# Kernel optimization log

Measured on AMD Instinct MI355X. Metric: run time of the kernel, lower is better.

## Reference

```python
import jax, jax.numpy as jnp
import numpy as np

N = 50000
E = 800000
D_IN, D_HID, D_OUT = 128, 128, 64


def setup_inputs() -> dict:
    key = jax.random.key(0)
    ks = jax.random.split(key, 8)
    x = jax.random.normal(ks[0], (N, D_IN), dtype=jnp.float32)
    edge_index = jax.random.randint(ks[1], (2, E), 0, N, dtype=jnp.int64)
    # SAGEConv params: lin_l (neighbors, with bias), lin_r (root, no bias)
    s1 = 1.0 / np.sqrt(D_IN)
    s2 = 1.0 / np.sqrt(D_HID)
    W1_l = jax.random.uniform(ks[2], (D_IN, D_HID), jnp.float32, -s1, s1)
    b1 = jnp.zeros((D_HID,), jnp.float32)
    W1_r = jax.random.uniform(ks[3], (D_IN, D_HID), jnp.float32, -s1, s1)
    W2_l = jax.random.uniform(ks[4], (D_HID, D_OUT), jnp.float32, -s2, s2)
    b2 = jnp.zeros((D_OUT,), jnp.float32)
    W2_r = jax.random.uniform(ks[5], (D_HID, D_OUT), jnp.float32, -s2, s2)
    return {"x": x, "edge_index": edge_index, "W1_l": W1_l, "b1": b1,
            "W1_r": W1_r, "W2_l": W2_l, "b2": b2, "W2_r": W2_r}


def _sage_conv(x, src, dst, Wl, b, Wr, num_nodes):
    # mean aggregation over incoming edges (src -> dst)
    msgs = x[src]                                              # [E, d]
    agg = jax.ops.segment_sum(msgs, dst, num_segments=num_nodes)
    cnt = jax.ops.segment_sum(jnp.ones((src.shape[0],), x.dtype), dst,
                              num_segments=num_nodes)
    mean = agg / jnp.clip(cnt, 1.0)[:, None]                   # [N, d]
    return mean @ Wl + b + x @ Wr


def reference(x, edge_index, W1_l, b1, W1_r, W2_l, b2, W2_r):
    src, dst = edge_index[0], edge_index[1]
    n = x.shape[0]
    h = jax.nn.relu(_sage_conv(x, src, dst, W1_l, b1, W1_r, n))
    # dropout p=0.5 is identity in eval mode (training=False)
    return _sage_conv(h, src, dst, W2_l, b2, W2_r, n)
```

## Files before the change

### kernel.cpp

```cpp
#include <hip/hip_runtime.h>
#include <hip/hip_bf16.h>

typedef __hip_bfloat16 bf16;
typedef __attribute__((ext_vector_type(8))) short short8;
typedef __attribute__((ext_vector_type(4))) float floatx4;
typedef __attribute__((ext_vector_type(2))) float floatx2;
typedef unsigned short u16;
typedef unsigned char u8;

#define NNODES 50000
#define NEDGES 800000
#define D_IN  128
#define D_HID 128
#define D_OUT 64
#define NBLK  ((NNODES + 255) / 256)

__device__ __forceinline__ float bfbits2f(unsigned int u) {
    return __uint_as_float(u << 16);
}
__device__ __forceinline__ float b2f(bf16 v) { return __bfloat162float(v); }
__device__ __forceinline__ unsigned short f2bfbits(float f) {
    bf16 b = __float2bfloat16(f);
    return *(unsigned short*)&b;
}
__device__ __forceinline__ u8 f2fp8(float f) {
    return (u8)(__builtin_amdgcn_cvt_pk_fp8_f32(f, 0.f, 0, false) & 0xFF);
}
__device__ __forceinline__ float ld(const void* p, long long idx, int isf32) {
    if (isf32) return ((const float*)p)[idx];
    return b2f(((const bf16*)p)[idx]);
}

__global__ void k_setup(int* __restrict__ cnt, int n,
                        const unsigned int* __restrict__ ei_words,
                        const unsigned int* __restrict__ w_words,
                        int* __restrict__ flags,
                        const void* __restrict__ x,
                        const void* __restrict__ W1l, const void* __restrict__ W1r,
                        const void* __restrict__ W2l, const void* __restrict__ W2r,
                        bf16* __restrict__ p1l, bf16* __restrict__ p1r,
                        bf16* __restrict__ p2l, bf16* __restrict__ p2r,
                        unsigned int* __restrict__ x8) {
    int b = blockIdx.x;
    if (b < 128) {
        if (b == 0) {
            __shared__ int cnt_zero, cnt_bf;
            if (threadIdx.x == 0) { cnt_zero = 0; cnt_bf = 0; }
            __syncthreads();
            int t = threadIdx.x;
            unsigned int we = ei_words[2 * t + 1];
            if (we == 0u) atomicAdd(&cnt_zero, 1);
            unsigned int ww = w_words[t];
            unsigned int lowexp = (ww >> 7) & 0xFFu;
            if (lowexp >= 0x60u && lowexp <= 0x7Bu) atomicAdd(&cnt_bf, 1);
            __syncthreads();
            if (threadIdx.x == 0) {
                flags[0] = (cnt_zero >= 240) ? 1 : 0;
                flags[1] = (cnt_bf >= 192) ? 0 : 1;
            }
        }
        int i = b * blockDim.x + threadIdx.x;
        int stride = 128 * blockDim.x;
        for (; i < n; i += stride) cnt[i] = 0;
        return;
    }
    __shared__ int cnt_bf2;
    if (threadIdx.x == 0) cnt_bf2 = 0;
    __syncthreads();
    {
        unsigned int ww = w_words[threadIdx.x];
        unsigned int lowexp = (ww >> 7) & 0xFFu;
        if (lowexp >= 0x60u && lowexp <= 0x7Bu) atomicAdd(&cnt_bf2, 1);
    }
    __syncthreads();
    int isf32 = (cnt_bf2 >= 192) ? 0 : 1;
    if (b < 152) {
        int t = (b - 128) * 256 + threadIdx.x;
        if (t >= 6144) return;
        const void* Wm; bf16* dst; int NT; int base;
        if (t < 2048)      { Wm = W1l; dst = p1l; NT = 8; base = t; }
        else if (t < 4096) { Wm = W1r; dst = p1r; NT = 8; base = t - 2048; }
        else if (t < 5120) { Wm = W2l; dst = p2l; NT = 4; base = t - 4096; }
        else               { Wm = W2r; dst = p2r; NT = 4; base = t - 5120; }
        int lane = base & 63;
        int kt = (base >> 6) & 3;
        int nt = base >> 8;
        int Nmat = NT * 16;
        int krow = kt * 32 + ((lane >> 4) * 8);
        int col = nt * 16 + (lane & 15);
        #pragma unroll
        for (int j = 0; j < 8; j++) {
            float v = ld(Wm, (long long)(krow + j) * Nmat + col, isf32);
            dst[(((nt * 4 + kt) * 64 + lane) * 8) + j] = __float2bfloat16(v);
        }
        return;
    }
    const long long NU32 = (long long)NNODES * D_IN / 4;
    long long i = (long long)(b - 152) * 256 + threadIdx.x;
    long long stride = (long long)(gridDim.x - 152) * 256;
    if (isf32) {
        const float4* xf = (const float4*)x;
        for (; i < NU32; i += stride) {
            float4 f = xf[i];
            unsigned int w0 = __builtin_amdgcn_cvt_pk_fp8_f32(f.x, f.y, 0, false);
            w0 = __builtin_amdgcn_cvt_pk_fp8_f32(f.z, f.w, w0, true);
            x8[i] = w0;
        }
    } else {
        const ushort4* xb = (const ushort4*)x;
        for (; i < NU32; i += stride) {
            ushort4 s = xb[i];
            float f0 = bfbits2f(s.x), f1 = bfbits2f(s.y);
            float f2 = bfbits2f(s.z), f3 = bfbits2f(s.w);
            unsigned int w0 = __builtin_amdgcn_cvt_pk_fp8_f32(f0, f1, 0, false);
            w0 = __builtin_amdgcn_cvt_pk_fp8_f32(f2, f3, w0, true);
            x8[i] = w0;
        }
    }
}

__global__ void k_edges(const int* __restrict__ ei, const int* __restrict__ flags,
                        u16* __restrict__ src16, unsigned int* __restrict__ drpack,
                        int* __restrict__ cnt) {
    int e = blockIdx.x * blockDim.x + threadIdx.x;
    if (e >= NEDGES) return;
    int s, d;
    if (flags[0]) { s = ei[2 * e]; d = ei[2 * (NEDGES + e)]; }
    else          { s = ei[e];     d = ei[NEDGES + e]; }
    src16[e] = (u16)s;
    int rank = atomicAdd(&cnt[d], 1);
    drpack[e] = ((unsigned int)rank << 16) | (unsigned int)d;
}

__global__ void k_scan_a(const int* __restrict__ cnt, int* __restrict__ excl,
                         int* __restrict__ bsum) {
    __shared__ int s[256];
    int t = threadIdx.x;
    int i = blockIdx.x * 256 + t;
    int v = (i < NNODES) ? cnt[i] : 0;
    s[t] = v;
    __syncthreads();
    for (int off = 1; off < 256; off <<= 1) {
        int u = (t >= off) ? s[t - off] : 0;
        __syncthreads();
        s[t] += u;
        __syncthreads();
    }
    if (i < NNODES) excl[i] = s[t] - v;
    if (t == 255) bsum[blockIdx.x] = s[255];
}

__global__ void k_scan_bc(const int* __restrict__ excl, const int* __restrict__ bsum,
                          int* __restrict__ row_start) {
    __shared__ int s[256];
    __shared__ int bo;
    int t = threadIdx.x;
    int v = (t < NBLK) ? bsum[t] : 0;
    s[t] = v;
    __syncthreads();
    for (int off = 1; off < 256; off <<= 1) {
        int u = (t >= off) ? s[t - off] : 0;
        __syncthreads();
        s[t] += u;
        __syncthreads();
    }
    if (t == 0) bo = s[blockIdx.x] - bsum[blockIdx.x];
    __syncthreads();
    int i = blockIdx.x * 256 + t;
    if (i < NNODES) row_start[i] = bo + excl[i];
    if (i == 0) row_start[NNODES] = NEDGES;
}

__global__ void k_scatter(const u16* __restrict__ src16,
                          const unsigned int* __restrict__ drpack,
                          const int* __restrict__ row_start,
                          u16* __restrict__ csr16) {
    int e = blockIdx.x * blockDim.x + threadIdx.x;
    if (e >= NEDGES) return;
    unsigned int dp = drpack[e];
    int d = (int)(dp & 0xFFFFu);
    int r = (int)(dp >> 16);
    csr16[row_start[d] + r] = src16[e];
}

__device__ __forceinline__ void g16m(const unsigned int* __restrict__ x8w, int my,
                                     int j, int cnt2, int h, int c,
                                     float& a0, float& a1, float& a2, float& a3) {
    int jb = j + h * 8;
    int i0 = __shfl(my, jb + 0), i1 = __shfl(my, jb + 1);
    int i2 = __shfl(my, jb + 2), i3 = __shfl(my, jb + 3);
    int i4 = __shfl(my, jb + 4), i5 = __shfl(my, jb + 5);
    int i6 = __shfl(my, jb + 6), i7 = __shfl(my, jb + 7);
    unsigned int u0 = x8w[((unsigned)i0 << 5) + c];
    unsigned int u1 = x8w[((unsigned)i1 << 5) + c];
    unsigned int u2 = x8w[((unsigned)i2 << 5) + c];
    unsigned int u3 = x8w[((unsigned)i3 << 5) + c];
    unsigned int u4 = x8w[((unsigned)i4 << 5) + c];
    unsigned int u5 = x8w[((unsigned)i5 << 5) + c];
    unsigned int u6 = x8w[((unsigned)i6 << 5) + c];
    unsigned int u7 = x8w[((unsigned)i7 << 5) + c];
    float m0 = (jb + 0 < cnt2) ? 1.f : 0.f;
    float m1 = (jb + 1 < cnt2) ? 1.f : 0.f;
    float m2 = (jb + 2 < cnt2) ? 1.f : 0.f;
    float m3 = (jb + 3 < cnt2) ? 1.f : 0.f;
    float m4 = (jb + 4 < cnt2) ? 1.f : 0.f;
    float m5 = (jb + 5 < cnt2) ? 1.f : 0.f;
    float m6 = (jb + 6 < cnt2) ? 1.f : 0.f;
    float m7 = (jb + 7 < cnt2) ? 1.f : 0.f;
    floatx2 l0 = __builtin_amdgcn_cvt_pk_f32_fp8(u0, false);
    floatx2 h0 = __builtin_amdgcn_cvt_pk_f32_fp8(u0, true);
    floatx2 l1 = __builtin_amdgcn_cvt_pk_f32_fp8(u1, false);
    floatx2 h1 = __builtin_amdgcn_cvt_pk_f32_fp8(u1, true);
    floatx2 l2 = __builtin_amdgcn_cvt_pk_f32_fp8(u2, false);
    floatx2 h2 = __builtin_amdgcn_cvt_pk_f32_fp8(u2, true);
    floatx2 l3 = __builtin_amdgcn_cvt_pk_f32_fp8(u3, false);
    floatx2 h3 = __builtin_amdgcn_cvt_pk_f32_fp8(u3, true);
    floatx2 l4 = __builtin_amdgcn_cvt_pk_f32_fp8(u4, false);
    floatx2 h4 = __builtin_amdgcn_cvt_pk_f32_fp8(u4, true);
    floatx2 l5 = __builtin_amdgcn_cvt_pk_f32_fp8(u5, false);
    floatx2 h5 = __builtin_amdgcn_cvt_pk_f32_fp8(u5, true);
    floatx2 l6 = __builtin_amdgcn_cvt_pk_f32_fp8(u6, false);
    floatx2 h6 = __builtin_amdgcn_cvt_pk_f32_fp8(u6, true);
    floatx2 l7 = __builtin_amdgcn_cvt_pk_f32_fp8(u7, false);
    floatx2 h7 = __builtin_amdgcn_cvt_pk_f32_fp8(u7, true);
    a0 += m0 * l0.x; a1 += m0 * l0.y; a2 += m0 * h0.x; a3 += m0 * h0.y;
    a0 += m1 * l1.x; a1 += m1 * l1.y; a2 += m1 * h1.x; a3 += m1 * h1.y;
    a0 += m2 * l2.x; a1 += m2 * l2.y; a2 += m2 * h2.x; a3 += m2 * h2.y;
    a0 += m3 * l3.x; a1 += m3 * l3.y; a2 += m3 * h3.x; a3 += m3 * h3.y;
    a0 += m4 * l4.x; a1 += m4 * l4.y; a2 += m4 * h4.x; a3 += m4 * h4.y;
    a0 += m5 * l5.x; a1 += m5 * l5.y; a2 += m5 * h5.x; a3 += m5 * h5.y;
    a0 += m6 * l6.x; a1 += m6 * l6.y; a2 += m6 * h6.x; a3 += m6 * h6.y;
    a0 += m7 * l7.x; a1 += m7 * l7.y; a2 += m7 * h7.x; a3 += m7 * h7.y;
}

__global__ __launch_bounds__(512) void k_l1fused(
        const int* __restrict__ row_start, const u16* __restrict__ csr16,
        const void* __restrict__ x, const unsigned int* __restrict__ x8w,
        const int* __restrict__ flags,
        const bf16* __restrict__ p1l, const bf16* __restrict__ p1r,
        const bf16* __restrict__ p2l, const bf16* __restrict__ p2r,
        const void* __restrict__ b1, const void* __restrict__ b2v,
        u8* __restrict__ h28, float* __restrict__ hrf) {
    __shared__ bf16 ms[16][136];
    __shared__ bf16 xs[16][136];
    __shared__ bf16 hs[16][136];
    __shared__ u8 h2s8[16][72];
    __shared__ float hrs[16][68];
    int t = threadIdx.x;
    int w = t >> 6;
    int l = t & 63;
    int nb = blockIdx.x * 16;
    int isf32 = flags[1];
    int r0 = w * 2, r1 = r0 + 1;
    int h = l >> 5;
    int c = l & 31;

    int rsv = row_start[nb + r0 + min(l, 2)];
    int s0 = __shfl(rsv, 0), s1 = __shfl(rsv, 1), s2 = __shfl(rsv, 2);

    int ca = min(64, s1 - s0);
    int cb = min(64, s2 - s1);
    int mya = (l < ca) ? (int)csr16[s0 + l] : 0;
    int myb = (l < cb) ? (int)csr16[s1 + l] : 0;

    {
        long long ro0 = (long long)(nb + r0) * D_IN + 2 * l;
        long long ro1 = (long long)(nb + r1) * D_IN + 2 * l;
        unsigned int px0, px1;
        if (isf32) {
            float2 v0 = *(const float2*)((const float*)x + ro0);
            float2 v1 = *(const float2*)((const float*)x + ro1);
            px0 = ((unsigned int)f2bfbits(v0.y) << 16) | f2bfbits(v0.x);
            px1 = ((unsigned int)f2bfbits(v1.y) << 16) | f2bfbits(v1.x);
        } else {
            px0 = *(const unsigned int*)((const bf16*)x + ro0);
            px1 = *(const unsigned int*)((const bf16*)x + ro1);
        }
        *(unsigned int*)((bf16*)&xs[r0][0] + 2 * l) = px0;
        *(unsigned int*)((bf16*)&xs[r1][0] + 2 * l) = px1;
    }

    float aa0 = 0.f, aa1 = 0.f, aa2 = 0.f, aa3 = 0.f;
    float bb0 = 0.f, bb1 = 0.f, bb2 = 0.f, bb3 = 0.f;
    {
        int mx = max(ca, cb);
        for (int j = 0; j < mx; j += 16) {
            g16m(x8w, mya, j, ca, h, c, aa0, aa1, aa2, aa3);
            g16m(x8w, myb, j, cb, h, c, bb0, bb1, bb2, bb3);
        }
    }
    for (int base = s0 + 64; base < s1; base += 64) {
        int cnt2 = min(64, s1 - base);
        int my = (l < cnt2) ? (int)csr16[base + l] : 0;
        for (int j = 0; j < cnt2; j += 16) g16m(x8w, my, j, cnt2, h, c, aa0, aa1, aa2, aa3);
    }
    for (int base = s1 + 64; base < s2; base += 64) {
        int cnt2 = min(64, s2 - base);
        int my = (l < cnt2) ? (int)csr16[base + l] : 0;
        for (int j = 0; j < cnt2; j += 16) g16m(x8w, my, j, cnt2, h, c, bb0, bb1, bb2, bb3);
    }
    aa0 += __shfl_xor(aa0, 32); aa1 += __shfl_xor(aa1, 32);
    aa2 += __shfl_xor(aa2, 32); aa3 += __shfl_xor(aa3, 32);
    bb0 += __shfl_xor(bb0, 32); bb1 += __shfl_xor(bb1, 32);
    bb2 += __shfl_xor(bb2, 32); bb3 += __shfl_xor(bb3, 32);
    if (l < 32) {
        float inv = 1.0f / fmaxf((float)(s1 - s0), 1.0f);
        uint2 pk;
        pk.x = ((unsigned int)f2bfbits(aa1 * inv) << 16) | f2bfbits(aa0 * inv);
        pk.y = ((unsigned int)f2bfbits(aa3 * inv) << 16) | f2bfbits(aa2 * inv);
        *(uint2*)((bf16*)&ms[r0][0] + (c << 2)) = pk;
    } else {
        float inv = 1.0f / fmaxf((float)(s2 - s1), 1.0f);
        uint2 pk;
        pk.x = ((unsigned int)f2bfbits(bb1 * inv) << 16) | f2bfbits(bb0 * inv);
        pk.y = ((unsigned int)f2bfbits(bb3 * inv) << 16) | f2bfbits(bb2 * inv);
        *(uint2*)((bf16*)&ms[r1][0] + (c << 2)) = pk;
    }
    __syncthreads();

    int m = l & 15;
    int quad = l >> 4;
    floatx4 acc0 = {0.f, 0.f, 0.f, 0.f};
    #pragma unroll
    for (int kt = 0; kt < 4; kt++) {
        short8 amv = *(const short8*)&ms[m][kt * 32 + quad * 8];
        short8 axv = *(const short8*)&xs[m][kt * 32 + quad * 8];
        short8 bl0 = *(const short8*)(p1l + (((w * 4 + kt) * 64 + l) * 8));
        short8 br0 = *(const short8*)(p1r + (((w * 4 + kt) * 64 + l) * 8));
        acc0 = __builtin_amdgcn_mfma_f32_16x16x32_bf16(amv, bl0, acc0, 0, 0, 0);
        acc0 = __builtin_amdgcn_mfma_f32_16x16x32_bf16(axv, br0, acc0, 0, 0, 0);
    }
    int c0 = w * 16 + m;
    float bias0 = ld(b1, c0, isf32);
    #pragma unroll
    for (int r = 0; r < 4; r++) {
        hs[quad * 4 + r][c0] = __float2bfloat16(fmaxf(acc0[r] + bias0, 0.f));
    }
    __syncthreads();
    if (w < 4) {
        floatx4 acc2 = {0.f, 0.f, 0.f, 0.f};
        floatx4 acc3 = {0.f, 0.f, 0.f, 0.f};
        #pragma unroll
        for (int kt = 0; kt < 4; kt++) {
            short8 ah = *(const short8*)&hs[m][kt * 32 + quad * 8];
            short8 bw = *(const short8*)(p2l + (((w * 4 + kt) * 64 + l) * 8));
            short8 bz = *(const short8*)(p2r + (((w * 4 + kt) * 64 + l) * 8));
            acc2 = __builtin_amdgcn_mfma_f32_16x16x32_bf16(ah, bw, acc2, 0, 0, 0);
            acc3 = __builtin_amdgcn_mfma_f32_16x16x32_bf16(ah, bz, acc3, 0, 0, 0);
        }
        int c2 = w * 16 + m;
        float bias2 = ld(b2v, c2, isf32);
        #pragma unroll
        for (int r = 0; r < 4; r++) {
            h2s8[quad * 4 + r][c2] = f2fp8(acc2[r]);
            hrs[quad * 4 + r][c2] = acc3[r] + bias2;
        }
    }
    __syncthreads();
    if (t < 128) {
        int node = t >> 3, col0 = (t & 7) * 8;
        uint2 v = *(const uint2*)&h2s8[node][col0];
        *(uint2*)(h28 + (long long)(nb + node) * D_OUT + col0) = v;
    }
    if (t < 256) {
        int node = t >> 4, col0 = (t & 15) * 4;
        float4 v = *(const float4*)&hrs[node][col0];
        *(float4*)(hrf + (long long)(nb + node) * D_OUT + col0) = v;
    }
}

__device__ __forceinline__ void a16m(const unsigned int* __restrict__ h32, int my,
                                     int j, int cnt2, int g, int c,
                                     float& a0, float& a1, float& a2, float& a3) {
    int jj0 = j + g, jj1 = j + 4 + g, jj2 = j + 8 + g, jj3 = j + 12 + g;
    int i0 = __shfl(my, jj0);
    int i1 = __shfl(my, jj1);
    int i2 = __shfl(my, jj2);
    int i3 = __shfl(my, jj3);
    unsigned int u0 = h32[(size_t)i0 * 16 + c];
    unsigned int u1 = h32[(size_t)i1 * 16 + c];
    unsigned int u2 = h32[(size_t)i2 * 16 + c];
    unsigned int u3 = h32[(size_t)i3 * 16 + c];
    float m0 = (jj0 < cnt2) ? 1.f : 0.f;
    float m1 = (jj1 < cnt2) ? 1.f : 0.f;
    float m2 = (jj2 < cnt2) ? 1.f : 0.f;
    float m3 = (jj3 < cnt2) ? 1.f : 0.f;
    floatx2 l0 = __builtin_amdgcn_cvt_pk_f32_fp8(u0, false);
    floatx2 h0 = __builtin_amdgcn_cvt_pk_f32_fp8(u0, true);
    floatx2 l1 = __builtin_amdgcn_cvt_pk_f32_fp8(u1, false);
    floatx2 h1 = __builtin_amdgcn_cvt_pk_f32_fp8(u1, true);
    floatx2 l2 = __builtin_amdgcn_cvt_pk_f32_fp8(u2, false);
    floatx2 h2 = __builtin_amdgcn_cvt_pk_f32_fp8(u2, true);
    floatx2 l3 = __builtin_amdgcn_cvt_pk_f32_fp8(u3, false);
    floatx2 h3 = __builtin_amdgcn_cvt_pk_f32_fp8(u3, true);
    a0 += m0 * l0.x; a1 += m0 * l0.y; a2 += m0 * h0.x; a3 += m0 * h0.y;
    a0 += m1 * l1.x; a1 += m1 * l1.y; a2 += m1 * h1.x; a3 += m1 * h1.y;
    a0 += m2 * l2.x; a1 += m2 * l2.y; a2 += m2 * h2.x; a3 += m2 * h2.y;
    a0 += m3 * l3.x; a1 += m3 * l3.y; a2 += m3 * h3.x; a3 += m3 * h3.y;
}

__global__ void k_agg2g(const int* __restrict__ row_start, const u16* __restrict__ csr16,
                        const u8* __restrict__ h28, const float* __restrict__ hrf,
                        const int* __restrict__ flags, void* __restrict__ out) {
    int t = threadIdx.x;
    int lane = t & 63;
    int n0 = blockIdx.x * 8 + (t >> 6) * 2;
    int n1 = n0 + 1;
    int g = lane >> 4;
    int c = lane & 15;
    const unsigned int* h32 = (const unsigned int*)h28;

    int rsv = row_start[n0 + min(lane, 2)];
    int s0 = __shfl(rsv, 0), s1 = __shfl(rsv, 1), s2 = __shfl(rsv, 2);
    int ca = min(64, s1 - s0);
    int cb = min(64, s2 - s1);
    int mya = (lane < ca) ? (int)csr16[s0 + lane] : 0;
    int myb = (lane < cb) ? (int)csr16[s1 + lane] : 0;

    float4 hr = {0.f, 0.f, 0.f, 0.f};
    if (lane < 32) {
        int nn = (lane < 16) ? n0 : n1;
        hr = *(const float4*)&hrf[(size_t)nn * D_OUT + (c << 2)];
    }

    float a0 = 0.f, a1 = 0.f, a2 = 0.f, a3 = 0.f;
    float b0 = 0.f, b1 = 0.f, b2 = 0.f, b3 = 0.f;
    {
        int mx = max(ca, cb);
        for (int j = 0; j < mx; j += 16) {
            a16m(h32, mya, j, ca, g, c, a0, a1, a2, a3);
            a16m(h32, myb, j, cb, g, c, b0, b1, b2, b3);
        }
    }
    for (int base = s0 + 64; base < s1; base += 64) {
        int cnt2 = min(64, s1 - base);
        int my = (lane < cnt2) ? (int)csr16[base + lane] : 0;
        for (int j = 0; j < cnt2; j += 16) a16m(h32, my, j, cnt2, g, c, a0, a1, a2, a3);
    }
    for (int base = s1 + 64; base < s2; base += 64) {
        int cnt2 = min(64, s2 - base);
        int my = (lane < cnt2) ? (int)csr16[base + lane] : 0;
        for (int j = 0; j < cnt2; j += 16) a16m(h32, my, j, cnt2, g, c, b0, b1, b2, b3);
    }
    a0 += __shfl_xor(a0, 32); a0 += __shfl_xor(a0, 16);
    a1 += __shfl_xor(a1, 32); a1 += __shfl_xor(a1, 16);
    a2 += __shfl_xor(a2, 32); a2 += __shfl_xor(a2, 16);
    a3 += __shfl_xor(a3, 32); a3 += __shfl_xor(a3, 16);
    b0 += __shfl_xor(b0, 32); b0 += __shfl_xor(b0, 16);
    b1 += __shfl_xor(b1, 32); b1 += __shfl_xor(b1, 16);
    b2 += __shfl_xor(b2, 32); b2 += __shfl_xor(b2, 16);
    b3 += __shfl_xor(b3, 32); b3 += __shfl_xor(b3, 16);
    if (lane < 16) {
        float inv = 1.0f / fmaxf((float)(s1 - s0), 1.0f);
        float o0 = a0 * inv + hr.x;
        float o1 = a1 * inv + hr.y;
        float o2 = a2 * inv + hr.z;
        float o3 = a3 * inv + hr.w;
        if (flags[1]) {
            float4 v = {o0, o1, o2, o3};
            *(float4*)((float*)out + (size_t)n0 * D_OUT + (c << 2)) = v;
        } else {
            uint2 v;
            v.x = ((unsigned int)f2bfbits(o1) << 16) | f2bfbits(o0);
            v.y = ((unsigned int)f2bfbits(o3) << 16) | f2bfbits(o2);
            *(uint2*)((bf16*)out + (size_t)n0 * D_OUT + (c << 2)) = v;
        }
    } else if (lane < 32) {
        float inv = 1.0f / fmaxf((float)(s2 - s1), 1.0f);
        float o0 = b0 * inv + hr.x;
        float o1 = b1 * inv + hr.y;
        float o2 = b2 * inv + hr.z;
        float o3 = b3 * inv + hr.w;
        if (flags[1]) {
            float4 v = {o0, o1, o2, o3};
            *(float4*)((float*)out + (size_t)n1 * D_OUT + (c << 2)) = v;
        } else {
            uint2 v;
            v.x = ((unsigned int)f2bfbits(o1) << 16) | f2bfbits(o0);
            v.y = ((unsigned int)f2bfbits(o3) << 16) | f2bfbits(o2);
            *(uint2*)((bf16*)out + (size_t)n1 * D_OUT + (c << 2)) = v;
        }
    }
}

extern "C" void kernel_launch(void* const* d_in, const int* in_sizes, int n_in,
                              void* d_out, int out_size, void* d_ws, size_t ws_size,
                              hipStream_t stream) {
    const void* x   = d_in[0];
    const int*  ei  = (const int*)d_in[1];
    const void* W1l = d_in[2];
    const void* b1  = d_in[3];
    const void* W1r = d_in[4];
    const void* W2l = d_in[5];
    const void* b2v = d_in[6];
    const void* W2r = d_in[7];

    const int N = NNODES;
    const int E = NEDGES;

    int*          flags     = (int*)d_ws;
    u16*          src16     = (u16*)(flags + 4);
    unsigned int* drpack    = (unsigned int*)(src16 + E);
    int*          cnt       = (int*)(drpack + E);
    int*          excl      = cnt + N;
    int*          bsum      = excl + N;
    int*          row_start = bsum + 256;
    u16*          csr16     = (u16*)(row_start + (N + 16));
    bf16*         p1l       = (bf16*)(csr16 + E);
    bf16*         p1r       = p1l + 16384;
    bf16*         p2l       = p1r + 16384;
    bf16*         p2r       = p2l + 8192;
    unsigned int* x8        = (unsigned int*)(p2r + 8192);
    u8*           h28       = (u8*)(x8 + (size_t)N * D_IN / 4);
    float*        hrf       = (float*)(h28 + (size_t)N * D_OUT);

    k_setup<<<152 + 1024, 256, 0, stream>>>(cnt, N, (const unsigned int*)ei,
                                            (const unsigned int*)W1l, flags, x,
                                            W1l, W1r, W2l, W2r,
                                            p1l, p1r, p2l, p2r, x8);
    k_edges<<<(E + 255) / 256, 256, 0, stream>>>(ei, flags, src16, drpack, cnt);
    k_scan_a<<<NBLK, 256, 0, stream>>>(cnt, excl, bsum);
    k_scan_bc<<<NBLK, 256, 0, stream>>>(excl, bsum, row_start);
    k_scatter<<<(E + 255) / 256, 256, 0, stream>>>(src16, drpack, row_start, csr16);
    k_l1fused<<<N / 16, 512, 0, stream>>>(row_start, csr16, x, x8, flags,
                                          p1l, p1r, p2l, p2r, b1, b2v, h28, hrf);
    k_agg2g<<<N / 8, 256, 0, stream>>>(row_start, csr16, h28, hrf, flags, d_out);
}
```

Before: 196.2 us.

## Pad CSR rows to multiples of 16 with a zero sentinel row

```diff
diff --git a/kernel.cpp b/kernel.cpp
--- a/kernel.cpp
+++ b/kernel.cpp
@@ -14,6 +14,8 @@
 #define D_HID 128
 #define D_OUT 64
 #define NBLK  ((NNODES + 255) / 256)
+#define ZROW  NNODES
+#define CSRP_U16 (NEDGES + 16 * NNODES)
 
 __device__ __forceinline__ float bfbits2f(unsigned int u) {
     return __uint_as_float(u << 16);
@@ -40,7 +42,7 @@
                         const void* __restrict__ W2l, const void* __restrict__ W2r,
                         bf16* __restrict__ p1l, bf16* __restrict__ p1r,
                         bf16* __restrict__ p2l, bf16* __restrict__ p2r,
-                        unsigned int* __restrict__ x8) {
+                        unsigned int* __restrict__ x8, u8* __restrict__ h28) {
     int b = blockIdx.x;
     if (b < 128) {
         if (b == 0) {
@@ -58,6 +60,9 @@
                 flags[0] = (cnt_zero >= 240) ? 1 : 0;
                 flags[1] = (cnt_bf >= 192) ? 0 : 1;
             }
+        }
+        if (b == 1 && threadIdx.x < 16) {
+            ((unsigned int*)(h28 + (size_t)ZROW * D_OUT))[threadIdx.x] = 0u;
         }
         int i = b * blockDim.x + threadIdx.x;
         int stride = 128 * blockDim.x;
@@ -95,12 +100,14 @@
         }
         return;
     }
-    const long long NU32 = (long long)NNODES * D_IN / 4;
+    const long long NU32  = (long long)NNODES * D_IN / 4;
+    const long long NU32P = NU32 + D_IN / 4;
     long long i = (long long)(b - 152) * 256 + threadIdx.x;
     long long stride = (long long)(gridDim.x - 152) * 256;
     if (isf32) {
         const float4* xf = (const float4*)x;
-        for (; i < NU32; i += stride) {
+        for (; i < NU32P; i += stride) {
+            if (i >= NU32) { x8[i] = 0u; continue; }
             float4 f = xf[i];
             unsigned int w0 = __builtin_amdgcn_cvt_pk_fp8_f32(f.x, f.y, 0, false);
             w0 = __builtin_amdgcn_cvt_pk_fp8_f32(f.z, f.w, w0, true);
@@ -108,7 +115,8 @@
         }
     } else {
         const ushort4* xb = (const ushort4*)x;
-        for (; i < NU32; i += stride) {
+        for (; i < NU32P; i += stride) {
+            if (i >= NU32) { x8[i] = 0u; continue; }
             ushort4 s = xb[i];
             float f0 = bfbits2f(s.x), f1 = bfbits2f(s.y);
             float f2 = bfbits2f(s.z), f3 = bfbits2f(s.w);
@@ -133,12 +141,13 @@
 }
 
 __global__ void k_scan_a(const int* __restrict__ cnt, int* __restrict__ excl,
-                         int* __restrict__ bsum) {
+                         int* __restrict__ bsum, unsigned int* __restrict__ csrp32) {
     __shared__ int s[256];
     int t = threadIdx.x;
     int i = blockIdx.x * 256 + t;
     int v = (i < NNODES) ? cnt[i] : 0;
-    s[t] = v;
+    int vp = (v + 15) & ~15;
+    s[t] = vp;
     __syncthreads();
     for (int off = 1; off < 256; off <<= 1) {
         int u = (t >= off) ? s[t - off] : 0;
@@ -146,8 +155,11 @@
         s[t] += u;
         __syncthreads();
     }
-    if (i < NNODES) excl[i] = s[t] - v;
+    if (i < NNODES) excl[i] = s[t] - vp;
     if (t == 255) bsum[blockIdx.x] = s[255];
+    const int NCP = CSRP_U16 / 2;
+    for (int idx = blockIdx.x * 256 + t; idx < NCP; idx += NBLK * 256)
+        csrp32[idx] = 0xC350C350u;
 }
 
 __global__ void k_scan_bc(const int* __restrict__ excl, const int* __restrict__ bsum,
@@ -168,7 +180,7 @@
     __syncthreads();
     int i = blockIdx.x * 256 + t;
     if (i < NNODES) row_start[i] = bo + excl[i];
-    if (i == 0) row_start[NNODES] = NEDGES;
+    if (blockIdx.x == 0 && t == 0) row_start[NNODES] = s[NBLK - 1];
 }
 
 __global__ void k_scatter(const u16* __restrict__ src16,
@@ -183,14 +195,15 @@
     csr16[row_start[d] + r] = src16[e];
 }
 
-__device__ __forceinline__ void g16m(const unsigned int* __restrict__ x8w, int my,
-                                     int j, int cnt2, int h, int c,
+__device__ __forceinline__ void g16r(const u16* __restrict__ csr,
+                                     const unsigned int* __restrict__ x8w,
+                                     int base, int h, int c,
                                      float& a0, float& a1, float& a2, float& a3) {
-    int jb = j + h * 8;
-    int i0 = __shfl(my, jb + 0), i1 = __shfl(my, jb + 1);
-    int i2 = __shfl(my, jb + 2), i3 = __shfl(my, jb + 3);
-    int i4 = __shfl(my, jb + 4), i5 = __shfl(my, jb + 5);
-    int i6 = __shfl(my, jb + 6), i7 = __shfl(my, jb + 7);
+    uint4 iv = *(const uint4*)(csr + base + h * 8);
+    int i0 = (int)(iv.x & 0xFFFFu), i1 = (int)(iv.x >> 16);
+    int i2 = (int)(iv.y & 0xFFFFu), i3 = (int)(iv.y >> 16);
+    int i4 = (int)(iv.z & 0xFFFFu), i5 = (int)(iv.z >> 16);
+    int i6 = (int)(iv.w & 0xFFFFu), i7 = (int)(iv.w >> 16);
     unsigned int u0 = x8w[((unsigned)i0 << 5) + c];
     unsigned int u1 = x8w[((unsigned)i1 << 5) + c];
     unsigned int u2 = x8w[((unsigned)i2 << 5) + c];
@@ -199,14 +212,6 @@
     unsigned int u5 = x8w[((unsigned)i5 << 5) + c];
     unsigned int u6 = x8w[((unsigned)i6 << 5) + c];
     unsigned int u7 = x8w[((unsigned)i7 << 5) + c];
-    float m0 = (jb + 0 < cnt2) ? 1.f : 0.f;
-    float m1 = (jb + 1 < cnt2) ? 1.f : 0.f;
-    float m2 = (jb + 2 < cnt2) ? 1.f : 0.f;
-    float m3 = (jb + 3 < cnt2) ? 1.f : 0.f;
-    float m4 = (jb + 4 < cnt2) ? 1.f : 0.f;
-    float m5 = (jb + 5 < cnt2) ? 1.f : 0.f;
-    float m6 = (jb + 6 < cnt2) ? 1.f : 0.f;
-    float m7 = (jb + 7 < cnt2) ? 1.f : 0.f;
     floatx2 l0 = __builtin_amdgcn_cvt_pk_f32_fp8(u0, false);
     floatx2 h0 = __builtin_amdgcn_cvt_pk_f32_fp8(u0, true);
     floatx2 l1 = __builtin_amdgcn_cvt_pk_f32_fp8(u1, false);
@@ -223,18 +228,15 @@
     floatx2 h6 = __builtin_amdgcn_cvt_pk_f32_fp8(u6, true);
     floatx2 l7 = __builtin_amdgcn_cvt_pk_f32_fp8(u7, false);
     floatx2 h7 = __builtin_amdgcn_cvt_pk_f32_fp8(u7, true);
-    a0 += m0 * l0.x; a1 += m0 * l0.y; a2 += m0 * h0.x; a3 += m0 * h0.y;
-    a0 += m1 * l1.x; a1 += m1 * l1.y; a2 += m1 * h1.x; a3 += m1 * h1.y;
-    a0 += m2 * l2.x; a1 += m2 * l2.y; a2 += m2 * h2.x; a3 += m2 * h2.y;
-    a0 += m3 * l3.x; a1 += m3 * l3.y; a2 += m3 * h3.x; a3 += m3 * h3.y;
-    a0 += m4 * l4.x; a1 += m4 * l4.y; a2 += m4 * h4.x; a3 += m4 * h4.y;
-    a0 += m5 * l5.x; a1 += m5 * l5.y; a2 += m5 * h5.x; a3 += m5 * h5.y;
-    a0 += m6 * l6.x; a1 += m6 * l6.y; a2 += m6 * h6.x; a3 += m6 * h6.y;
-    a0 += m7 * l7.x; a1 += m7 * l7.y; a2 += m7 * h7.x; a3 += m7 * h7.y;
+    a0 += l0.x + l1.x + l2.x + l3.x + l4.x + l5.x + l6.x + l7.x;
+    a1 += l0.y + l1.y + l2.y + l3.y + l4.y + l5.y + l6.y + l7.y;
+    a2 += h0.x + h1.x + h2.x + h3.x + h4.x + h5.x + h6.x + h7.x;
+    a3 += h0.y + h1.y + h2.y + h3.y + h4.y + h5.y + h6.y + h7.y;
 }
 
 __global__ __launch_bounds__(512) void k_l1fused(
         const int* __restrict__ row_start, const u16* __restrict__ csr16,
+        const int* __restrict__ cnt,
         const void* __restrict__ x, const unsigned int* __restrict__ x8w,
         const int* __restrict__ flags,
         const bf16* __restrict__ p1l, const bf16* __restrict__ p1r,
@@ -257,11 +259,8 @@
 
     int rsv = row_start[nb + r0 + min(l, 2)];
     int s0 = __shfl(rsv, 0), s1 = __shfl(rsv, 1), s2 = __shfl(rsv, 2);
-
-    int ca = min(64, s1 - s0);
-    int cb = min(64, s2 - s1);
-    int mya = (l < ca) ? (int)csr16[s0 + l] : 0;
-    int myb = (l < cb) ? (int)csr16[s1 + l] : 0;
+    int cw = cnt[nb + r0 + min(l, 1)];
+    int da = __shfl(cw, 0), db = __shfl(cw, 1);
 
     {
         long long ro0 = (long long)(nb + r0) * D_IN + 2 * l;
@@ -282,35 +281,27 @@
 
     float aa0 = 0.f, aa1 = 0.f, aa2 = 0.f, aa3 = 0.f;
     float bb0 = 0.f, bb1 = 0.f, bb2 = 0.f, bb3 = 0.f;
-    {
-        int mx = max(ca, cb);
-        for (int j = 0; j < mx; j += 16) {
-            g16m(x8w, mya, j, ca, h, c, aa0, aa1, aa2, aa3);
-            g16m(x8w, myb, j, cb, h, c, bb0, bb1, bb2, bb3);
-        }
-    }
-    for (int base = s0 + 64; base < s1; base += 64) {
-        int cnt2 = min(64, s1 - base);
-        int my = (l < cnt2) ? (int)csr16[base + l] : 0;
-        for (int j = 0; j < cnt2; j += 16) g16m(x8w, my, j, cnt2, h, c, aa0, aa1, aa2, aa3);
-    }
-    for (int base = s1 + 64; base < s2; base += 64) {
-        int cnt2 = min(64, s2 - base);
-        int my = (l < cnt2) ? (int)csr16[base + l] : 0;
-        for (int j = 0; j < cnt2; j += 16) g16m(x8w, my, j, cnt2, h, c, bb0, bb1, bb2, bb3);
-    }
+    int pa = s1 - s0, pb = s2 - s1;
+    int mn = min(pa, pb);
+    int j = 0;
+    for (; j < mn; j += 16) {
+        g16r(csr16, x8w, s0 + j, h, c, aa0, aa1, aa2, aa3);
+        g16r(csr16, x8w, s1 + j, h, c, bb0, bb1, bb2, bb3);
+    }
+    for (; j < pa; j += 16) g16r(csr16, x8w, s0 + j, h, c, aa0, aa1, aa2, aa3);
+    for (; j < pb; j += 16) g16r(csr16, x8w, s1 + j, h, c, bb0, bb1, bb2, bb3);
     aa0 += __shfl_xor(aa0, 32); aa1 += __shfl_xor(aa1, 32);
     aa2 += __shfl_xor(aa2, 32); aa3 += __shfl_xor(aa3, 32);
     bb0 += __shfl_xor(bb0, 32); bb1 += __shfl_xor(bb1, 32);
     bb2 += __shfl_xor(bb2, 32); bb3 += __shfl_xor(bb3, 32);
     if (l < 32) {
-        float inv = 1.0f / fmaxf((float)(s1 - s0), 1.0f);
+        float inv = 1.0f / fmaxf((float)da, 1.0f);
         uint2 pk;
         pk.x = ((unsigned int)f2bfbits(aa1 * inv) << 16) | f2bfbits(aa0 * inv);
         pk.y = ((unsigned int)f2bfbits(aa3 * inv) << 16) | f2bfbits(aa2 * inv);
         *(uint2*)((bf16*)&ms[r0][0] + (c << 2)) = pk;
     } else {
-        float inv = 1.0f / fmaxf((float)(s2 - s1), 1.0f);
+        float inv = 1.0f / fmaxf((float)db, 1.0f);
         uint2 pk;
         pk.x = ((unsigned int)f2bfbits(bb1 * inv) << 16) | f2bfbits(bb0 * inv);
         pk.y = ((unsigned int)f2bfbits(bb3 * inv) << 16) | f2bfbits(bb2 * inv);
@@ -369,22 +360,21 @@
     }
 }
 
-__device__ __forceinline__ void a16m(const unsigned int* __restrict__ h32, int my,
-                                     int j, int cnt2, int g, int c,
+__device__ __forceinline__ void a16r(const u16* __restrict__ csr,
+                                     const unsigned int* __restrict__ h32,
+                                     int base, int g, int c,
                                      float& a0, float& a1, float& a2, float& a3) {
-    int jj0 = j + g, jj1 = j + 4 + g, jj2 = j + 8 + g, jj3 = j + 12 + g;
-    int i0 = __shfl(my, jj0);
-    int i1 = __shfl(my, jj1);
-    int i2 = __shfl(my, jj2);
-    int i3 = __shfl(my, jj3);
+    uint4 iva = *(const uint4*)(csr + base);
+    uint4 ivb = *(const uint4*)(csr + base + 8);
+    unsigned int sh = (unsigned int)(g & 1) << 4;
+    int i0 = (int)((((g & 2) ? iva.y : iva.x) >> sh) & 0xFFFFu);
+    int i1 = (int)((((g & 2) ? iva.w : iva.z) >> sh) & 0xFFFFu);
+    int i2 = (int)((((g & 2) ? ivb.y : ivb.x) >> sh) & 0xFFFFu);
+    int i3 = (int)((((g & 2) ? ivb.w : ivb.z) >> sh) & 0xFFFFu);
     unsigned int u0 = h32[(size_t)i0 * 16 + c];
     unsigned int u1 = h32[(size_t)i1 * 16 + c];
     unsigned int u2 = h32[(size_t)i2 * 16 + c];
     unsigned int u3 = h32[(size_t)i3 * 16 + c];
-    float m0 = (jj0 < cnt2) ? 1.f : 0.f;
-    float m1 = (jj1 < cnt2) ? 1.f : 0.f;
-    float m2 = (jj2 < cnt2) ? 1.f : 0.f;
-    float m3 = (jj3 < cnt2) ? 1.f : 0.f;
     floatx2 l0 = __builtin_amdgcn_cvt_pk_f32_fp8(u0, false);
     floatx2 h0 = __builtin_amdgcn_cvt_pk_f32_fp8(u0, true);
     floatx2 l1 = __builtin_amdgcn_cvt_pk_f32_fp8(u1, false);
@@ -393,13 +383,14 @@
     floatx2 h2 = __builtin_amdgcn_cvt_pk_f32_fp8(u2, true);
     floatx2 l3 = __builtin_amdgcn_cvt_pk_f32_fp8(u3, false);
     floatx2 h3 = __builtin_amdgcn_cvt_pk_f32_fp8(u3, true);
-    a0 += m0 * l0.x; a1 += m0 * l0.y; a2 += m0 * h0.x; a3 += m0 * h0.y;
-    a0 += m1 * l1.x; a1 += m1 * l1.y; a2 += m1 * h1.x; a3 += m1 * h1.y;
-    a0 += m2 * l2.x; a1 += m2 * l2.y; a2 += m2 * h2.x; a3 += m2 * h2.y;
-    a0 += m3 * l3.x; a1 += m3 * l3.y; a2 += m3 * h3.x; a3 += m3 * h3.y;
+    a0 += l0.x + l1.x + l2.x + l3.x;
+    a1 += l0.y + l1.y + l2.y + l3.y;
+    a2 += h0.x + h1.x + h2.x + h3.x;
+    a3 += h0.y + h1.y + h2.y + h3.y;
 }
 
 __global__ void k_agg2g(const int* __restrict__ row_start, const u16* __restrict__ csr16,
+                        const int* __restrict__ cnt,
                         const u8* __restrict__ h28, const float* __restrict__ hrf,
                         const int* __restrict__ flags, void* __restrict__ out) {
     int t = threadIdx.x;
@@ -412,10 +403,8 @@
 
     int rsv = row_start[n0 + min(lane, 2)];
     int s0 = __shfl(rsv, 0), s1 = __shfl(rsv, 1), s2 = __shfl(rsv, 2);
-    int ca = min(64, s1 - s0);
-    int cb = min(64, s2 - s1);
-    int mya = (lane < ca) ? (int)csr16[s0 + lane] : 0;
-    int myb = (lane < cb) ? (int)csr16[s1 + lane] : 0;
+    int cw = cnt[n0 + min(lane, 1)];
+    int da = __shfl(cw, 0), db = __shfl(cw, 1);
 
     float4 hr = {0.f, 0.f, 0.f, 0.f};
     if (lane < 32) {
@@ -425,23 +414,16 @@
 
     float a0 = 0.f, a1 = 0.f, a2 = 0.f, a3 = 0.f;
     float b0 = 0.f, b1 = 0.f, b2 = 0.f, b3 = 0.f;
-    {
-        int mx = max(ca, cb);
-        for (int j = 0; j < mx; j += 16) {
-            a16m(h32, mya, j, ca, g, c, a0, a1, a2, a3);
-            a16m(h32, myb, j, cb, g, c, b0, b1, b2, b3);
-        }
-    }
-    for (int base = s0 + 64; base < s1; base += 64) {
-        int cnt2 = min(64, s1 - base);
-        int my = (lane < cnt2) ? (int)csr16[base + lane] : 0;
-        for (int j = 0; j < cnt2; j += 16) a16m(h32, my, j, cnt2, g, c, a0, a1, a2, a3);
-    }
-    for (int base = s1 + 64; base < s2; base += 64) {
-        int cnt2 = min(64, s2 - base);
-        int my = (lane < cnt2) ? (int)csr16[base + lane] : 0;
-        for (int j = 0; j < cnt2; j += 16) a16m(h32, my, j, cnt2, g, c, b0, b1, b2, b3);
-    }
+    int pa = s1 - s0, pb = s2 - s1;
+    int mn = min(pa, pb);
+    int j = 0;
+    for (; j < mn; j += 16) {
+        a16r(csr16, h32, s0 + j, g, c, a0, a1, a2, a3);
+        a16r(csr16, h32, s1 + j, g, c, b0, b1, b2, b3);
+    }
+    for (; j < pa; j += 16) a16r(csr16, h32, s0 + j, g, c, a0, a1, a2, a3);
+    for (; j < pb; j += 16) a16r(csr16, h32, s1 + j, g, c, b0, b1, b2, b3);
+
     a0 += __shfl_xor(a0, 32); a0 += __shfl_xor(a0, 16);
     a1 += __shfl_xor(a1, 32); a1 += __shfl_xor(a1, 16);
     a2 += __shfl_xor(a2, 32); a2 += __shfl_xor(a2, 16);
@@ -451,7 +433,7 @@
     b2 += __shfl_xor(b2, 32); b2 += __shfl_xor(b2, 16);
     b3 += __shfl_xor(b3, 32); b3 += __shfl_xor(b3, 16);
     if (lane < 16) {
-        float inv = 1.0f / fmaxf((float)(s1 - s0), 1.0f);
+        float inv = 1.0f / fmaxf((float)da, 1.0f);
         float o0 = a0 * inv + hr.x;
         float o1 = a1 * inv + hr.y;
         float o2 = a2 * inv + hr.z;
@@ -466,7 +448,7 @@
             *(uint2*)((bf16*)out + (size_t)n0 * D_OUT + (c << 2)) = v;
         }
     } else if (lane < 32) {
-        float inv = 1.0f / fmaxf((float)(s2 - s1), 1.0f);
+        float inv = 1.0f / fmaxf((float)db, 1.0f);
         float o0 = b0 * inv + hr.x;
         float o1 = b1 * inv + hr.y;
         float o2 = b2 * inv + hr.z;
@@ -506,23 +488,23 @@
     int*          bsum      = excl + N;
     int*          row_start = bsum + 256;
     u16*          csr16     = (u16*)(row_start + (N + 16));
-    bf16*         p1l       = (bf16*)(csr16 + E);
+    bf16*         p1l       = (bf16*)(csr16 + CSRP_U16);
     bf16*         p1r       = p1l + 16384;
     bf16*         p2l       = p1r + 16384;
     bf16*         p2r       = p2l + 8192;
     unsigned int* x8        = (unsigned int*)(p2r + 8192);
-    u8*           h28       = (u8*)(x8 + (size_t)N * D_IN / 4);
-    float*        hrf       = (float*)(h28 + (size_t)N * D_OUT);
+    u8*           h28       = (u8*)(x8 + (size_t)(N + 1) * D_IN / 4);
+    float*        hrf       = (float*)(h28 + (size_t)(N + 1) * D_OUT);
 
     k_setup<<<152 + 1024, 256, 0, stream>>>(cnt, N, (const unsigned int*)ei,
                                             (const unsigned int*)W1l, flags, x,
                                             W1l, W1r, W2l, W2r,
-                                            p1l, p1r, p2l, p2r, x8);
+                                            p1l, p1r, p2l, p2r, x8, h28);
     k_edges<<<(E + 255) / 256, 256, 0, stream>>>(ei, flags, src16, drpack, cnt);
-    k_scan_a<<<NBLK, 256, 0, stream>>>(cnt, excl, bsum);
+    k_scan_a<<<NBLK, 256, 0, stream>>>(cnt, excl, bsum, (unsigned int*)csr16);
     k_scan_bc<<<NBLK, 256, 0, stream>>>(excl, bsum, row_start);
     k_scatter<<<(E + 255) / 256, 256, 0, stream>>>(src16, drpack, row_start, csr16);
-    k_l1fused<<<N / 16, 512, 0, stream>>>(row_start, csr16, x, x8, flags,
+    k_l1fused<<<N / 16, 512, 0, stream>>>(row_start, csr16, cnt, x, x8, flags,
                                           p1l, p1r, p2l, p2r, b1, b2v, h28, hrf);
-    k_agg2g<<<N / 8, 256, 0, stream>>>(row_start, csr16, h28, hrf, flags, d_out);
-}
+    k_agg2g<<<N / 8, 256, 0, stream>>>(row_start, csr16, cnt, h28, hrf, flags, d_out);
+}
```

Measured after the change: 202.0 us. 1.03x slower.
